# Optimization experiments

Measured on AMD Instinct MI355X. Metric: run time of the kernel, lower is better.

Reference implementation:

```python
import jax, jax.numpy as jnp
import numpy as np

D = 32   # manifold_dim
H = 128  # hidden_dim
B = 32   # batch


def setup_inputs() -> dict:
    key = jax.random.key(0)
    ks = jax.random.split(key, 13)
    def lin(k, fan_in, shape):
        # torch nn.Linear default init: U(-1/sqrt(fan_in), 1/sqrt(fan_in))
        return jax.random.uniform(k, shape, jnp.float32, -1.0, 1.0) / np.float32(np.sqrt(fan_in))
    return {
        "points": jax.random.normal(ks[0], (B, D), jnp.float32),
        # metric_network: Linear(D,H) -> ReLU -> Linear(H, D*D)
        "mw1": lin(ks[1], D, (D, H)), "mb1": lin(ks[2], D, (H,)),
        "mw2": lin(ks[3], H, (H, D * D)), "mb2": lin(ks[4], H, (D * D,)),
        # christoffel_network: Linear(D+3,H) -> Tanh -> Linear(H,1)  (scalar output per (i,j,k))
        "cw1": lin(ks[5], D + 3, (D + 3, H)), "cb1": lin(ks[6], D + 3, (H,)),
        "cw2": lin(ks[7], H, (H,)), "cb2": lin(ks[8], H, ()),
        # ricci_network: Linear(2D+1, 2H) -> ReLU -> Linear(2H, 1)
        "rw1": lin(ks[9], 2 * D + 1, (2 * D + 1, 2 * H)), "rb1": lin(ks[10], 2 * D + 1, (2 * H,)),
        "rw2": lin(ks[11], 2 * H, (2 * H,)), "rb2": lin(ks[12], 2 * H, ()),
    }


def _forward(points, mw1, mb1, mw2, mb2, cw1, cb1, cw2, cb2, rw1, rb1, rw2, rb2):
    b, d = points.shape
    # metric tensor g: [b, d, d]
    metric = (jax.nn.relu(points @ mw1 + mb1) @ mw2 + mb2).reshape(b, d, d)

    # Christoffel MLP input per (i,j,k): cat([points, g_ij, g_jk, g_ki]) -> [b,d,d,d,d+3]
    gij = jnp.broadcast_to(metric[:, :, :, None], (b, d, d, d))                       # g[i,j]
    gjk = jnp.broadcast_to(metric[:, None, :, :], (b, d, d, d))                       # g[j,k]
    gki = jnp.broadcast_to(jnp.swapaxes(metric, 1, 2)[:, :, None, :], (b, d, d, d))   # g[k,i]
    pts = jnp.broadcast_to(points[:, None, None, None, :], (b, d, d, d, d))
    cin = jnp.concatenate([pts, gij[..., None], gjk[..., None], gki[..., None]], axis=-1)
    ch = jnp.tanh(jnp.einsum('bijkf,fh->bijkh', cin, cw1) + cb1)
    christoffel = jnp.einsum('bijkh,h->bijk', ch, cw2) + cb2                          # [b,d,d,d]

    # Ricci MLP input per (i,j): cat([points, g_ij, Gamma_ij[:]]) -> [b,d,d,2d+1]
    pts2 = jnp.broadcast_to(points[:, None, None, :], (b, d, d, d))
    rin = jnp.concatenate([pts2, metric[..., None], christoffel], axis=-1)
    rh = jax.nn.relu(jnp.einsum('bijf,fh->bijh', rin, rw1) + rb1)
    ricci = jnp.einsum('bijh,h->bij', rh, rw2) + rb2                                  # [b,d,d]
    return ricci


def reference(points, mw1, mb1, mw2, mb2, cw1, cb1, cw2, cb2, rw1, rb1, rw2, rb2):
    return _forward(points, mw1, mb1, mw2, mb2, cw1, cb1, cw2, cb2, rw1, rb1, rw2, rb2)
```

## Files before the change

kernel.cpp:

```cpp
#include <hip/hip_runtime.h>

#define D 32
#define H 128
#define TN 1024
#define TRANGE 6.0f

typedef float v2f __attribute__((ext_vector_type(2)));

__global__ __launch_bounds__(256) void setup_kernel(
    const float* __restrict__ points,
    const float* __restrict__ mw1, const float* __restrict__ mb1,
    const float* __restrict__ mw2, const float* __restrict__ mb2,
    const float* __restrict__ cw1, const float* __restrict__ cb1,
    const float* __restrict__ rw1, const float* __restrict__ rb1,
    float* __restrict__ metric, float4* __restrict__ cpk4,
    float* __restrict__ rbase)
{
    __shared__ float p[D];
    __shared__ float h1[H];
    const int blk = blockIdx.x;
    const int b   = blk >> 3;
    const int q   = blk & 7;
    const int t   = threadIdx.x;
    if (t < D) p[t] = points[b * D + t];
    __syncthreads();

    if (t < H) {
        float acc = mb1[t];
        #pragma unroll
        for (int d = 0; d < D; ++d) acc = fmaf(p[d], mw1[d * H + t], acc);
        h1[t] = fmaxf(acc, 0.0f);
    }

    if (q == 0 && t < H) {
        constexpr float S = (float)TN / (2.0f * TRANGE);
        float cacc = cb1[t];
        #pragma unroll
        for (int d = 0; d < D; ++d) cacc = fmaf(p[d], cw1[d * H + t], cacc);
        cpk4[b * H + t] = make_float4(S * cacc + (float)(TN / 2),
                                      S * cw1[32 * H + t],
                                      S * cw1[33 * H + t],
                                      S * cw1[34 * H + t]);
    }
    if (q == 1) {
        float racc = rb1[t];
        #pragma unroll
        for (int d = 0; d < D; ++d) racc = fmaf(p[d], rw1[d * 256 + t], racc);
        rbase[b * 256 + t] = racc;
    }
    __syncthreads();

    if (t < 128) {
        const int m = q * 128 + t;
        float acc = mb2[m];
        #pragma unroll 8
        for (int h = 0; h < H; ++h) acc = fmaf(h1[h], mw2[h * 1024 + m], acc);
        metric[b * 1024 + m] = acc;
    }
}

__global__ __launch_bounds__(256) void christoffel_kernel(
    const float* __restrict__ metric,
    const float4* __restrict__ cpk4, const float* __restrict__ cw2,
    const float* __restrict__ cb2,
    float* __restrict__ gamma)
{
    __shared__ float M[D * D];
    __shared__ float2 tab[TN];
    const int blk = blockIdx.x;
    const int b   = blk >> 6;
    const int i   = (blk >> 1) & 31;
    const int jh  = blk & 1;
    const int t   = threadIdx.x;

    constexpr float hstep = 2.0f * TRANGE / (float)TN;
    constexpr float Kc = 2.8853900817779268f;
    #pragma unroll
    for (int qq = 0; qq < TN / 256; ++qq) {
        const int idx = qq * 256 + t;
        const float x0 = -TRANGE + idx * hstep;
        const float e0 = __builtin_amdgcn_exp2f(Kc * x0);
        const float v0 = 1.0f - 2.0f * __builtin_amdgcn_rcpf(e0 + 1.0f);
        const float e1 = __builtin_amdgcn_exp2f(Kc * (x0 + hstep));
        const float v1 = 1.0f - 2.0f * __builtin_amdgcn_rcpf(e1 + 1.0f);
        tab[idx] = make_float2(v0, v1 - v0);
    }
    #pragma unroll
    for (int qq = 0; qq < 4; ++qq) M[qq * 256 + t] = metric[b * 1024 + qq * 256 + t];
    __syncthreads();

    const int j  = jh * 16 + (t >> 4);
    const int k0 = (t & 15) * 2;

    const float gij = M[i * 32 + j];
    const float gjk0 = M[j * 32 + k0], gjk1 = M[j * 32 + k0 + 1];
    const float gki0 = M[k0 * 32 + i], gki1 = M[(k0 + 1) * 32 + i];
    float acc0 = 0.0f, acc1 = 0.0f;

    const float4* __restrict__ cp = cpk4 + b * H;

    #pragma unroll 4
    for (int h = 0; h < H; ++h) {
        const float4 c = cp[h];
        const float w = cw2[h];
        const float pre = fmaf(gij, c.y, c.x);
        float u0 = fmaf(gki0, c.w, fmaf(gjk0, c.z, pre));
        float u1 = fmaf(gki1, c.w, fmaf(gjk1, c.z, pre));
        u0 = fminf(fmaxf(u0, 0.0f), 1023.0f);
        u1 = fminf(fmaxf(u1, 0.0f), 1023.0f);
        const int i0 = (int)u0;
        const int i1 = (int)u1;
        const float fr0 = u0 - (float)i0;
        const float fr1 = u1 - (float)i1;
        const float2 p0 = tab[i0];
        const float2 p1 = tab[i1];
        acc0 = fmaf(fmaf(fr0, p0.y, p0.x), w, acc0);
        acc1 = fmaf(fmaf(fr1, p1.y, p1.x), w, acc1);
    }

    const float bias = cb2[0];
    v2f res; res.x = acc0 + bias; res.y = acc1 + bias;
    *((v2f*)(gamma + ((b * 32 + i) * 32 + j) * 32 + k0)) = res;
}

__global__ __launch_bounds__(256) void ricci_kernel(
    const float* __restrict__ metric, const float* __restrict__ rbase,
    const float* __restrict__ rw1, const float* __restrict__ rw2,
    const float* __restrict__ rb2,
    const float* __restrict__ gamma,
    float* __restrict__ out)
{
    __shared__ float red[4][16];
    const int blk = blockIdx.x;
    const int bi  = blk >> 1;
    const int b   = blk >> 6;
    const int i   = (blk >> 1) & 31;
    const int jh  = blk & 1;
    const int t   = threadIdx.x;

    float w[33];
    #pragma unroll
    for (int f = 0; f < 33; ++f) w[f] = rw1[(32 + f) * 256 + t];
    const float rbv   = rbase[b * 256 + t];
    const float wo    = rw2[t];
    const float rbias = rb2[0];

    const float4* __restrict__ G4   = (const float4*)(gamma + bi * 1024 + jh * 512);
    const float*  __restrict__ Mrow = metric + b * 1024 + i * 32 + jh * 16;

    const int wid  = t >> 6;
    const int lane = t & 63;

    #pragma unroll 2
    for (int jp = 0; jp < 8; ++jp) {
        float pp[2];
        #pragma unroll
        for (int s = 0; s < 2; ++s) {
            const int jj = jp * 2 + s;
            v2f hA = (v2f)(0.0f), hB = (v2f)(0.0f);
            #pragma unroll
            for (int k4 = 0; k4 < 8; ++k4) {
                const float4 g = G4[jj * 8 + k4];
                v2f glo; glo.x = g.x; glo.y = g.y;
                v2f ghi; ghi.x = g.z; ghi.y = g.w;
                v2f wlo; wlo.x = w[k4 * 4 + 1]; wlo.y = w[k4 * 4 + 2];
                v2f whi; whi.x = w[k4 * 4 + 3]; whi.y = w[k4 * 4 + 4];
                hA = glo * wlo + hA;
                hB = ghi * whi + hB;
            }
            const float hid = fmaf(Mrow[jj], w[0], rbv) + (hA.x + hA.y) + (hB.x + hB.y);
            pp[s] = fmaxf(hid, 0.0f) * wo;
        }
        const float t0 = pp[0] + __shfl_xor(pp[0], 1);
        const float t1 = pp[1] + __shfl_xor(pp[1], 1);
        float z = (lane & 1) ? t1 : t0;
        #pragma unroll
        for (int off = 2; off < 64; off <<= 1) z += __shfl_xor(z, off);
        if (lane < 2) red[wid][jp * 2 + lane] = z;
    }
    __syncthreads();
    if (t < 16) out[bi * 32 + jh * 16 + t] = red[0][t] + red[1][t] + red[2][t] + red[3][t] + rbias;
}

extern "C" void kernel_launch(void* const* d_in, const int* in_sizes, int n_in,
                              void* d_out, int out_size, void* d_ws, size_t ws_size,
                              hipStream_t stream) {
    const float* points = (const float*)d_in[0];
    const float* mw1 = (const float*)d_in[1];
    const float* mb1 = (const float*)d_in[2];
    const float* mw2 = (const float*)d_in[3];
    const float* mb2 = (const float*)d_in[4];
    const float* cw1 = (const float*)d_in[5];
    const float* cb1 = (const float*)d_in[6];
    const float* cw2 = (const float*)d_in[7];
    const float* cb2 = (const float*)d_in[8];
    const float* rw1 = (const float*)d_in[9];
    const float* rb1 = (const float*)d_in[10];
    const float* rw2 = (const float*)d_in[11];
    const float* rb2 = (const float*)d_in[12];
    float* out = (float*)d_out;

    char* ws = (char*)d_ws;
    float*  metric = (float*)(ws);
    float4* cpk4   = (float4*)(ws + 131072);
    float*  rbase  = (float*)(ws + 196608);
    float*  gamma  = (float*)(ws + 262144);

    setup_kernel<<<256, 256, 0, stream>>>(points, mw1, mb1, mw2, mb2,
                                          cw1, cb1, rw1, rb1,
                                          metric, cpk4, rbase);
    christoffel_kernel<<<2048, 256, 0, stream>>>(metric, cpk4, cw2, cb2, gamma);
    ricci_kernel<<<2048, 256, 0, stream>>>(metric, rbase, rw1, rw2, rb2, gamma, out);
}
```

Before: 54.63 us.

## Split tanh evaluation between a lookup table and direct exp/rcp per hidden unit

```diff
diff --git a/kernel.cpp b/kernel.cpp
--- a/kernel.cpp
+++ b/kernel.cpp
@@ -2,19 +2,21 @@
 
 #define D 32
 #define H 128
-#define TN 1024
+#define TN 256
 #define TRANGE 6.0f
 
 typedef float v2f __attribute__((ext_vector_type(2)));
+typedef float v8f __attribute__((ext_vector_type(8)));
 
 __global__ __launch_bounds__(256) void setup_kernel(
     const float* __restrict__ points,
     const float* __restrict__ mw1, const float* __restrict__ mb1,
     const float* __restrict__ mw2, const float* __restrict__ mb2,
     const float* __restrict__ cw1, const float* __restrict__ cb1,
+    const float* __restrict__ cw2, const float* __restrict__ cb2,
     const float* __restrict__ rw1, const float* __restrict__ rb1,
-    float* __restrict__ metric, float4* __restrict__ cpk4,
-    float* __restrict__ rbase)
+    float* __restrict__ metric, v8f* __restrict__ cpkT, v8f* __restrict__ cpkX,
+    float* __restrict__ rbase, float* __restrict__ cc)
 {
     __shared__ float p[D];
     __shared__ float h1[H];
@@ -33,20 +35,40 @@
     }
 
     if (q == 0 && t < H) {
-        constexpr float S = (float)TN / (2.0f * TRANGE);
-        float cacc = cb1[t];
-        #pragma unroll
-        for (int d = 0; d < D; ++d) cacc = fmaf(p[d], cw1[d * H + t], cacc);
-        cpk4[b * H + t] = make_float4(S * cacc + (float)(TN / 2),
-                                      S * cw1[32 * H + t],
-                                      S * cw1[33 * H + t],
-                                      S * cw1[34 * H + t]);
+        constexpr float S  = (float)TN / (2.0f * TRANGE);
+        constexpr float Kc = 2.8853900817779268f;
+        const int h = t;
+        float cacc = cb1[h];
+        #pragma unroll
+        for (int d = 0; d < D; ++d) cacc = fmaf(p[d], cw1[d * H + h], cacc);
+        const float a1 = cw1[32 * H + h];
+        const float a2 = cw1[33 * H + h];
+        const float a3 = cw1[34 * H + h];
+        const float w  = cw2[h];
+        v8f c;
+        if ((h & 1) == 0) {
+            c[0] = S * cacc + (float)(TN / 2);
+            c[1] = S * a1; c[2] = S * a2; c[3] = S * a3;
+            c[4] = w; c[5] = 0.0f; c[6] = 0.0f; c[7] = 0.0f;
+            cpkT[b * 64 + (h >> 1)] = c;
+        } else {
+            c[0] = Kc * cacc;
+            c[1] = Kc * a1; c[2] = Kc * a2; c[3] = Kc * a3;
+            c[4] = -2.0f * w; c[5] = 0.0f; c[6] = 0.0f; c[7] = 0.0f;
+            cpkX[b * 64 + (h >> 1)] = c;
+        }
     }
     if (q == 1) {
         float racc = rb1[t];
         #pragma unroll
         for (int d = 0; d < D; ++d) racc = fmaf(p[d], rw1[d * 256 + t], racc);
         rbase[b * 256 + t] = racc;
+    }
+    if (q == 2 && b == 0 && t < 64) {
+        float v = cw2[2 * t + 1];
+        #pragma unroll
+        for (int off = 32; off > 0; off >>= 1) v += __shfl_xor(v, off);
+        if (t == 0) cc[0] = v + cb2[0];
     }
     __syncthreads();
 
@@ -61,11 +83,10 @@
 
 __global__ __launch_bounds__(256) void christoffel_kernel(
     const float* __restrict__ metric,
-    const float4* __restrict__ cpk4, const float* __restrict__ cw2,
-    const float* __restrict__ cb2,
+    const v8f* __restrict__ cpkT, const v8f* __restrict__ cpkX,
+    const float* __restrict__ cc,
     float* __restrict__ gamma)
 {
-    __shared__ float M[D * D];
     __shared__ float2 tab[TN];
     const int blk = blockIdx.x;
     const int b   = blk >> 6;
@@ -75,50 +96,60 @@
 
     constexpr float hstep = 2.0f * TRANGE / (float)TN;
     constexpr float Kc = 2.8853900817779268f;
-    #pragma unroll
-    for (int qq = 0; qq < TN / 256; ++qq) {
-        const int idx = qq * 256 + t;
-        const float x0 = -TRANGE + idx * hstep;
+    if (t < TN) {
+        const float x0 = -TRANGE + t * hstep;
         const float e0 = __builtin_amdgcn_exp2f(Kc * x0);
         const float v0 = 1.0f - 2.0f * __builtin_amdgcn_rcpf(e0 + 1.0f);
         const float e1 = __builtin_amdgcn_exp2f(Kc * (x0 + hstep));
         const float v1 = 1.0f - 2.0f * __builtin_amdgcn_rcpf(e1 + 1.0f);
-        tab[idx] = make_float2(v0, v1 - v0);
-    }
-    #pragma unroll
-    for (int qq = 0; qq < 4; ++qq) M[qq * 256 + t] = metric[b * 1024 + qq * 256 + t];
-    __syncthreads();
+        tab[t] = make_float2(v0, v1 - v0);
+    }
 
     const int j  = jh * 16 + (t >> 4);
     const int k0 = (t & 15) * 2;
-
-    const float gij = M[i * 32 + j];
-    const float gjk0 = M[j * 32 + k0], gjk1 = M[j * 32 + k0 + 1];
-    const float gki0 = M[k0 * 32 + i], gki1 = M[(k0 + 1) * 32 + i];
+    const float* __restrict__ Mb = metric + b * 1024;
+    const float gij  = Mb[i * 32 + j];
+    const float gjk0 = Mb[j * 32 + k0];
+    const float gjk1 = Mb[j * 32 + k0 + 1];
+    const float gki0 = Mb[k0 * 32 + i];
+    const float gki1 = Mb[(k0 + 1) * 32 + i];
+    __syncthreads();
+
     float acc0 = 0.0f, acc1 = 0.0f;
-
-    const float4* __restrict__ cp = cpk4 + b * H;
+    const v8f* __restrict__ cpT = cpkT + b * 64;
+    const v8f* __restrict__ cpX = cpkX + b * 64;
 
     #pragma unroll 4
-    for (int h = 0; h < H; ++h) {
-        const float4 c = cp[h];
-        const float w = cw2[h];
-        const float pre = fmaf(gij, c.y, c.x);
-        float u0 = fmaf(gki0, c.w, fmaf(gjk0, c.z, pre));
-        float u1 = fmaf(gki1, c.w, fmaf(gjk1, c.z, pre));
-        u0 = fminf(fmaxf(u0, 0.0f), 1023.0f);
-        u1 = fminf(fmaxf(u1, 0.0f), 1023.0f);
-        const int i0 = (int)u0;
-        const int i1 = (int)u1;
-        const float fr0 = u0 - (float)i0;
-        const float fr1 = u1 - (float)i1;
-        const float2 p0 = tab[i0];
-        const float2 p1 = tab[i1];
-        acc0 = fmaf(fmaf(fr0, p0.y, p0.x), w, acc0);
-        acc1 = fmaf(fmaf(fr1, p1.y, p1.x), w, acc1);
-    }
-
-    const float bias = cb2[0];
+    for (int hp = 0; hp < 64; ++hp) {
+        const v8f ct = cpT[hp];
+        const v8f cx = cpX[hp];
+        {
+            const float pre = fmaf(gij, ct[1], ct[0]);
+            float u0 = fmaf(gki0, ct[3], fmaf(gjk0, ct[2], pre));
+            float u1 = fmaf(gki1, ct[3], fmaf(gjk1, ct[2], pre));
+            u0 = __builtin_amdgcn_fmed3f(u0, 0.0f, (float)(TN - 1));
+            u1 = __builtin_amdgcn_fmed3f(u1, 0.0f, (float)(TN - 1));
+            const int   i0 = (int)u0;
+            const int   i1 = (int)u1;
+            const float fr0 = u0 - (float)i0;
+            const float fr1 = u1 - (float)i1;
+            const float2 p0 = tab[i0];
+            const float2 p1 = tab[i1];
+            acc0 = fmaf(fmaf(fr0, p0.y, p0.x), ct[4], acc0);
+            acc1 = fmaf(fmaf(fr1, p1.y, p1.x), ct[4], acc1);
+        }
+        {
+            const float pre = fmaf(gij, cx[1], cx[0]);
+            const float x0 = fmaf(gki0, cx[3], fmaf(gjk0, cx[2], pre));
+            const float x1 = fmaf(gki1, cx[3], fmaf(gjk1, cx[2], pre));
+            const float r0 = __builtin_amdgcn_rcpf(__builtin_amdgcn_exp2f(x0) + 1.0f);
+            const float r1 = __builtin_amdgcn_rcpf(__builtin_amdgcn_exp2f(x1) + 1.0f);
+            acc0 = fmaf(r0, cx[4], acc0);
+            acc1 = fmaf(r1, cx[4], acc1);
+        }
+    }
+
+    const float bias = cc[0];
     v2f res; res.x = acc0 + bias; res.y = acc1 + bias;
     *((v2f*)(gamma + ((b * 32 + i) * 32 + j) * 32 + k0)) = res;
 }
@@ -201,14 +232,16 @@
     float* out = (float*)d_out;
 
     char* ws = (char*)d_ws;
-    float*  metric = (float*)(ws);
-    float4* cpk4   = (float4*)(ws + 131072);
-    float*  rbase  = (float*)(ws + 196608);
-    float*  gamma  = (float*)(ws + 262144);
+    float* metric = (float*)(ws);
+    v8f*   cpkT   = (v8f*)(ws + 131072);
+    v8f*   cpkX   = (v8f*)(ws + 196608);
+    float* rbase  = (float*)(ws + 262144);
+    float* cc     = (float*)(ws + 294912);
+    float* gamma  = (float*)(ws + 295168);
 
     setup_kernel<<<256, 256, 0, stream>>>(points, mw1, mb1, mw2, mb2,
-                                          cw1, cb1, rw1, rb1,
-                                          metric, cpk4, rbase);
-    christoffel_kernel<<<2048, 256, 0, stream>>>(metric, cpk4, cw2, cb2, gamma);
+                                          cw1, cb1, cw2, cb2, rw1, rb1,
+                                          metric, cpkT, cpkX, rbase, cc);
+    christoffel_kernel<<<2048, 256, 0, stream>>>(metric, cpkT, cpkX, cc, gamma);
     ricci_kernel<<<2048, 256, 0, stream>>>(metric, rbase, rw1, rw2, rb2, gamma, out);
 }
```

New measurement: 55.30 us. No clear change (+1.2%).
